# Performance work log

Measured on AMD Instinct MI355X. Metric: run time of the kernel, lower is better.

The kernel has to match this reference:

```python
import jax, jax.numpy as jnp
import numpy as np

NA = 3
ANCHORS = np.array([1.28967, 4.15014, 2.12714, 5.09344, 3.27212, 5.87423], dtype=np.float32)
OBJECT_SCALE = 5.0
NOOBJECT_SCALE = 1.0
CLASS_SCALE = 1.0
COORD_SCALE = 1.0
SIL_THRESH = 0.6
GAMMA = 0.5
EPS = 1e-7


def _iou_cxcywh(b1, b2):
    # b1, b2: [..., 4] as (cx, cy, w, h); broadcasting elementwise IoU
    mx = jnp.minimum(b1[..., 0] - b1[..., 2] * 0.5, b2[..., 0] - b2[..., 2] * 0.5)
    Mx = jnp.maximum(b1[..., 0] + b1[..., 2] * 0.5, b2[..., 0] + b2[..., 2] * 0.5)
    my = jnp.minimum(b1[..., 1] - b1[..., 3] * 0.5, b2[..., 1] - b2[..., 3] * 0.5)
    My = jnp.maximum(b1[..., 1] + b1[..., 3] * 0.5, b2[..., 1] + b2[..., 3] * 0.5)
    uw = Mx - mx
    uh = My - my
    cw = b1[..., 2] + b2[..., 2] - uw
    ch = b1[..., 3] + b2[..., 3] - uh
    inter = jnp.where((cw <= 0) | (ch <= 0), 0.0, cw * ch)
    union = b1[..., 2] * b1[..., 3] + b2[..., 2] * b2[..., 3] - inter
    return inter / union


def setup_inputs() -> dict:
    key = jax.random.key(0)
    k1, k2, k3, k4, k5 = jax.random.split(key, 5)
    nB, nC, nH, nW = 32, 80, 56, 56
    output = jax.random.normal(k1, (nB, NA * (5 + nC), nH, nW), dtype=jnp.float32)
    cxy = jax.random.uniform(k2, (nB, 50, 2), minval=0.02, maxval=0.98)
    wh = jax.random.uniform(k3, (nB, 50, 2), minval=0.05, maxval=0.6)
    target_boxes = jnp.concatenate([cxy, wh], axis=-1).astype(jnp.float32)
    target_cls = (jax.random.uniform(k4, (nB, 50, nC)) < 0.05).astype(jnp.float32)
    class_weight = jax.random.uniform(k5, (nC,), dtype=jnp.float32)
    return {"output": output, "target_boxes": target_boxes,
            "target_cls": target_cls, "class_weight": class_weight}


def reference(output, target_boxes, target_cls, class_weight):
    sg = jax.lax.stop_gradient
    anchors = jnp.asarray(ANCHORS)
    aw_all, ah_all = anchors[0::2], anchors[1::2]          # [nA]
    nB, _, nH, nW = output.shape
    nC = class_weight.shape[0]
    nA = NA
    out = output.reshape(nB, nA, 5 + nC, nH, nW)
    x = jax.nn.sigmoid(out[:, :, 0])                        # [nB,nA,nH,nW]
    y = jax.nn.sigmoid(out[:, :, 1])
    w = out[:, :, 2]
    h = out[:, :, 3]
    conf = jax.nn.sigmoid(out[:, :, 4])
    # class probs: [nB,nA,nH,nW,nC] (matches torch view/transpose to [nB*nA*nH*nW, nC])
    p_cls = jax.nn.sigmoid(jnp.transpose(out[:, :, 5:], (0, 1, 3, 4, 2)))

    grid_x = jnp.arange(nW, dtype=jnp.float32)[None, None, None, :]
    grid_y = jnp.arange(nH, dtype=jnp.float32)[None, None, :, None]
    # predicted boxes in grid units (detached, as torch uses .data)
    px = sg(x) + grid_x
    py = sg(y) + grid_y
    pw = jnp.exp(sg(w)) * aw_all[None, :, None, None]
    ph = jnp.exp(sg(h)) * ah_all[None, :, None, None]
    pred = jnp.stack([px, py, pw, ph], axis=-1).reshape(nB, nA * nH * nW, 4)

    # ---- build_targets (vectorized over (b, t, anchor*cell)) ----
    scale = jnp.array([nW, nH, nW, nH], dtype=jnp.float32)
    g = sg(target_boxes) * scale                            # [nB,50,4] grid units
    valid = target_boxes[:, :, 2] > 0                       # [nB,50]
    # IoU of every gt against every predicted box; max over gt -> silence mask
    ious = _iou_cxcywh(g[:, :, None, :], pred[:, None, :, :])  # [nB,50,nA*nH*nW]
    max_iou = jnp.max(jnp.where(valid[:, :, None], ious, 0.0), axis=1)
    conf_mask = jnp.where(max_iou > SIL_THRESH, 0.0, NOOBJECT_SCALE)  # [nB,nA*nH*nW]

    gx, gy, gw, gh = g[..., 0], g[..., 1], g[..., 2], g[..., 3]
    # best anchor by centered-box IoU: inter = min(w)*min(h)
    inter_a = jnp.minimum(aw_all, gw[..., None]) * jnp.minimum(ah_all, gh[..., None])
    union_a = aw_all * ah_all + (gw * gh)[..., None] - inter_a
    best_n = jnp.argmax(inter_a / union_a, axis=-1)         # [nB,50]

    gi = jnp.clip(gx.astype(jnp.int32), 0, nW - 1)
    gj = jnp.clip(gy.astype(jnp.int32), 0, nH - 1)
    b_idx = jnp.arange(nB)[:, None]
    flat = ((b_idx * nA + best_n) * nH + gj) * nW + gi      # [nB,50]
    total = nB * nA * nH * nW
    idx = jnp.where(valid, flat, total).reshape(-1)         # invalid -> out-of-range, dropped

    zeros = jnp.zeros((total,), dtype=jnp.float32)
    coord_mask = zeros.at[idx].set(1.0, mode="drop")
    conf_mask = conf_mask.reshape(-1).at[idx].set(OBJECT_SCALE, mode="drop")
    aw_b = aw_all[best_n]
    ah_b = ah_all[best_n]
    tx = zeros.at[idx].set((gx - gi.astype(jnp.float32)).reshape(-1), mode="drop")
    ty = zeros.at[idx].set((gy - gj.astype(jnp.float32)).reshape(-1), mode="drop")
    tw = zeros.at[idx].set(jnp.log(gw / aw_b).reshape(-1), mode="drop")
    th = zeros.at[idx].set(jnp.log(gh / ah_b).reshape(-1), mode="drop")
    pred_flat = pred.reshape(total, 4)
    pred_at = pred_flat[jnp.where(valid, flat, 0).reshape(-1)]  # [nB*50,4]
    iou_gt = _iou_cxcywh(g.reshape(-1, 4), pred_at)
    tconf = zeros.at[idx].set(iou_gt, mode="drop")
    tcls = jnp.zeros((total, nC), dtype=jnp.float32).at[idx].set(
        sg(target_cls).reshape(-1, nC), mode="drop")

    shp = (nB, nA, nH, nW)
    coord_mask = sg(coord_mask.reshape(shp))
    conf_mask = sg(conf_mask.reshape(shp))
    tx, ty, tw, th, tconf = (sg(t.reshape(shp)) for t in (tx, ty, tw, th, tconf))
    tcls = sg(tcls.reshape(nB, nA, nH, nW, nC))

    # ---- losses ----
    loss_x = 0.5 * COORD_SCALE * jnp.sum(coord_mask * (x - tx) ** 2)
    loss_y = 0.5 * COORD_SCALE * jnp.sum(coord_mask * (y - ty) ** 2)
    loss_w = 0.5 * COORD_SCALE * jnp.sum(coord_mask * (w - tw) ** 2)
    loss_h = 0.5 * COORD_SCALE * jnp.sum(coord_mask * (h - th) ** 2)
    # conf_mask is sqrt'ed then squared inside MSE -> equals conf_mask weighting
    loss_conf = 0.5 * jnp.sum(conf_mask * (conf - tconf) ** 2)

    # binary focal loss over cells selected by cls_mask (== coord_mask), size-averaged
    l1 = (1.0 - p_cls + EPS) ** GAMMA * jnp.log(p_cls + EPS) * jnp.exp(class_weight)
    l0 = (p_cls + EPS) ** GAMMA * jnp.log(1.0 - p_cls + EPS) * jnp.exp(1.0 - class_weight)
    per_el = tcls * l1 + (1.0 - tcls) * l0
    nsel = jnp.maximum(jnp.sum(coord_mask), 1.0)
    loss_cls = CLASS_SCALE * (-jnp.sum(coord_mask[..., None] * per_el) / nsel)

    return loss_x + loss_y + loss_w + loss_h + loss_conf + loss_cls
```

## Files before the change

### kernel.cpp

```cpp
#include <hip/hip_runtime.h>
#include <math.h>

#define NB 32
#define NA 3
#define NC 80
#define NH 56
#define NW 56
#define NT 50
#define HW (NH*NW)
#define CELLS_PER_B (NA*HW)
#define CH_PER_A (5+NC)
#define EPSF 1e-7f
#define NBX ((CELLS_PER_B + 255) / 256)
#define NBLK (NBX*NB)

__device__ __forceinline__ float fsig(float v) { return 1.0f / (1.0f + __expf(-v)); }

__global__ __launch_bounds__(256) void fused_kernel(const float* __restrict__ out,
                                                    const float* __restrict__ tb,
                                                    const float* __restrict__ tcls,
                                                    const float* __restrict__ cwt,
                                                    float4* __restrict__ part) {
    __shared__ float4 sp1[NT];
    __shared__ float2 sqf[NT];
    __shared__ int    s_obj[NT];
    __shared__ int    s_cnt;
    __shared__ float  redm[4], redc[4];

    const int b = blockIdx.y;
    const int tid = threadIdx.x;

    const float aw[3]  = {1.28967f, 2.12714f, 3.27212f};
    const float ah[3]  = {4.15014f, 5.09344f, 5.87423f};
    const float law[3] = {0.25438842f, 0.75477730f, 1.18543813f};
    const float lah[3] = {1.42314173f, 1.62795138f, 1.77057764f};

    if (tid == 0) s_cnt = 0;
    if (tid < NT) {
        float4 box = ((const float4*)tb)[b * NT + tid];
        if (box.z > 0.0f) {
            float gx = box.x * (float)NW;
            float gy = box.y * (float)NH;
            float gw = box.z * (float)NW;
            float gh = box.w * (float)NH;
            sp1[tid] = make_float4(gx - 0.5f * gw, gx + 0.5f * gw,
                                   gy - 0.5f * gh, gy + 0.5f * gh);
            int bn = 0; float best = -1.0f;
            #pragma unroll
            for (int k = 0; k < 3; ++k) {
                float inter = fminf(aw[k], gw) * fminf(ah[k], gh);
                float uni = aw[k] * ah[k] + gw * gh - inter;
                float r = inter / uni;
                if (r > best) { best = r; bn = k; }
            }
            int gi = (int)gx; gi = gi < 0 ? 0 : (gi > NW - 1 ? NW - 1 : gi);
            int gj = (int)gy; gj = gj < 0 ? 0 : (gj > NH - 1 ? NH - 1 : gj);
            int flat = (bn * NH + gj) * NW + gi;
            sqf[tid] = make_float2(0.375f * gw * gh, __int_as_float(flat));
        } else {
            sp1[tid] = make_float4(1e9f, -1e9f, 1e9f, -1e9f);
            sqf[tid] = make_float2(0.0f, __int_as_float(-1));
        }
    }
    __syncthreads();

    const int lc = blockIdx.x * 256 + tid;
    float lmain = 0.0f;

    if (lc < CELLS_PER_B) {
        const int a = lc / HW;
        const int rem = lc - a * HW;
        const int j = rem / NW;
        const int i = rem - j * NW;

        const float* base = out + (size_t)b * (NA * CH_PER_A * HW) + (size_t)(a * CH_PER_A) * HW + rem;
        float o0 = base[0];
        float o1 = base[HW];
        float o2 = base[2 * HW];
        float o3 = base[3 * HW];
        float o4 = base[4 * HW];

        float x = fsig(o0);
        float y = fsig(o1);
        float conf = fsig(o4);
        float pw = __expf(o2) * aw[a];
        float ph = __expf(o3) * ah[a];
        float px = x + (float)i;
        float py = y + (float)j;
        float px1 = px - 0.5f * pw, px2 = px + 0.5f * pw;
        float py1 = py - 0.5f * ph, py2 = py + 0.5f * ph;
        float qp = 0.375f * (pw * ph);

        bool sil = false;
        int tsel = -1;
        #pragma unroll 5
        for (int t = 0; t < NT; ++t) {
            float4 p1 = sp1[t];
            float2 qf = sqf[t];
            float iw = fminf(p1.y, px2) - fmaxf(p1.x, px1);
            float ih = fminf(p1.w, py2) - fmaxf(p1.z, py1);
            float in = fmaxf(iw, 0.f) * fmaxf(ih, 0.f);
            sil = sil || (in > qf.x + qp);
            if (__float_as_int(qf.y) == lc) tsel = t;
        }

        if (tsel >= 0) {
            float4 g1 = sp1[tsel];
            float gw = g1.y - g1.x, gh = g1.w - g1.z;
            float gx = 0.5f * (g1.x + g1.y), gy = 0.5f * (g1.z + g1.w);
            float tx = gx - (float)i, ty = gy - (float)j;
            float tw = __logf(gw) - law[a], th = __logf(gh) - lah[a];
            lmain += 0.5f * ((x - tx) * (x - tx) + (y - ty) * (y - ty) +
                             (o2 - tw) * (o2 - tw) + (o3 - th) * (o3 - th));
            float iw = fminf(g1.y, px2) - fmaxf(g1.x, px1);
            float ih = fminf(g1.w, py2) - fmaxf(g1.z, py1);
            float inter = fmaxf(iw, 0.f) * fmaxf(ih, 0.f);
            float uni = gw * gh + pw * ph - inter;
            float tconf = inter / uni;
            lmain += 2.5f * (conf - tconf) * (conf - tconf);

            int pos = atomicAdd(&s_cnt, 1);
            s_obj[pos] = (lc << 6) | tsel;
        } else {
            lmain += sil ? 0.0f : 0.5f * conf * conf;
        }
    }
    __syncthreads();

    const int cnt = s_cnt;
    float lcls = 0.0f;
    if (cnt > 0) {
        const int oo = tid / NC;
        const int c = tid - oo * NC;
        if (oo < 3) {
            float w = cwt[c];
            float ew1 = __expf(w);
            float ew0 = __expf(1.0f - w);
            for (int o0 = 0; o0 < cnt; o0 += 3) {
                int o = o0 + oo;
                if (o < cnt) {
                    int pk = s_obj[o];
                    int olc = pk >> 6;
                    int tsel = pk & 63;
                    int a = olc / HW;
                    int rem = olc - a * HW;
                    float p = fsig(out[(size_t)b * (NA * CH_PER_A * HW) +
                                       (size_t)(a * CH_PER_A + 5 + c) * HW + rem]);
                    float t = tcls[(size_t)(b * NT + tsel) * NC + c];
                    float l1 = sqrtf(1.0f - p + EPSF) * __logf(p + EPSF) * ew1;
                    float l0 = sqrtf(p + EPSF) * __logf(1.0f - p + EPSF) * ew0;
                    lcls += t * l1 + (1.0f - t) * l0;
                }
            }
        }
    }

    for (int off = 32; off > 0; off >>= 1) {
        lmain += __shfl_down(lmain, off, 64);
        lcls  += __shfl_down(lcls, off, 64);
    }
    if ((tid & 63) == 0) { redm[tid >> 6] = lmain; redc[tid >> 6] = lcls; }
    __syncthreads();
    if (tid == 0) {
        float m = redm[0] + redm[1] + redm[2] + redm[3];
        float c = redc[0] + redc[1] + redc[2] + redc[3];
        part[blockIdx.y * NBX + blockIdx.x] = make_float4(m, c, (float)cnt, 0.0f);
    }
}

__global__ __launch_bounds__(256) void finalize_kernel(const float4* __restrict__ part,
                                                       float* __restrict__ outp) {
    const int tid = threadIdx.x;
    float m = 0.0f, c = 0.0f, n = 0.0f;
    for (int i = tid; i < NBLK; i += 256) {
        float4 p = part[i];
        m += p.x; c += p.y; n += p.z;
    }
    for (int off = 32; off > 0; off >>= 1) {
        m += __shfl_down(m, off, 64);
        c += __shfl_down(c, off, 64);
        n += __shfl_down(n, off, 64);
    }
    __shared__ float rm[4], rc[4], rn[4];
    if ((tid & 63) == 0) { rm[tid >> 6] = m; rc[tid >> 6] = c; rn[tid >> 6] = n; }
    __syncthreads();
    if (tid == 0) {
        float ms = rm[0] + rm[1] + rm[2] + rm[3];
        float cs = rc[0] + rc[1] + rc[2] + rc[3];
        float ns = rn[0] + rn[1] + rn[2] + rn[3];
        float nsel = fmaxf(ns, 1.0f);
        outp[0] = ms - cs / nsel;
    }
}

extern "C" void kernel_launch(void* const* d_in, const int* in_sizes, int n_in,
                              void* d_out, int out_size, void* d_ws, size_t ws_size,
                              hipStream_t stream) {
    const float* output = (const float*)d_in[0];
    const float* tb     = (const float*)d_in[1];
    const float* tcls   = (const float*)d_in[2];
    const float* cwt    = (const float*)d_in[3];

    float4* part = (float4*)d_ws;

    fused_kernel<<<dim3(NBX, NB), 256, 0, stream>>>(output, tb, tcls, cwt, part);
    finalize_kernel<<<1, 256, 0, stream>>>(part, (float*)d_out);
}
```

Before: 20.19 us.

## Scatter target cell map in shared memory and issue class-prob loads early

Target-to-cell assignment now runs before the main IoU loop. Each target writes its index into a per-block shared map with atomicMax, which removes the per-cell comparison against every target's flat index inside the 50-iteration loop. Because the object list is known early, the first class-probability, target-class and class-weight loads are issued before the silence IoU loop, so their global-memory latency overlaps with that compute. The cost is two extra block barriers and some extra shared memory.

```diff
diff --git a/kernel.cpp b/kernel.cpp
--- a/kernel.cpp
+++ b/kernel.cpp
@@ -22,20 +22,41 @@
                                                     const float* __restrict__ cwt,
                                                     float4* __restrict__ part) {
     __shared__ float4 sp1[NT];
-    __shared__ float2 sqf[NT];
+    __shared__ float  sq[NT];
+    __shared__ int    s_map[256];
     __shared__ int    s_obj[NT];
     __shared__ int    s_cnt;
     __shared__ float  redm[4], redc[4];
 
     const int b = blockIdx.y;
     const int tid = threadIdx.x;
+    const int block_lo = blockIdx.x * 256;
+    const int lc = block_lo + tid;
+    const size_t bofs = (size_t)b * (NA * CH_PER_A * HW);
 
     const float aw[3]  = {1.28967f, 2.12714f, 3.27212f};
     const float ah[3]  = {4.15014f, 5.09344f, 5.87423f};
     const float law[3] = {0.25438842f, 0.75477730f, 1.18543813f};
     const float lah[3] = {1.42314173f, 1.62795138f, 1.77057764f};
 
+    const int a = lc / HW;
+    const int rem = lc - a * HW;
+    const int j = rem / NW;
+    const int i = rem - j * NW;
+    float o0 = 0.f, o1 = 0.f, o2 = 0.f, o3 = 0.f, o4 = 0.f;
+    const bool cv = (lc < CELLS_PER_B);
+    if (cv) {
+        const float* base = out + bofs + (size_t)(a * CH_PER_A) * HW + rem;
+        o0 = base[0];
+        o1 = base[HW];
+        o2 = base[2 * HW];
+        o3 = base[3 * HW];
+        o4 = base[4 * HW];
+    }
+
+    s_map[tid] = 0;
     if (tid == 0) s_cnt = 0;
+    int myflat = -1;
     if (tid < NT) {
         float4 box = ((const float4*)tb)[b * NT + tid];
         if (box.z > 0.0f) {
@@ -45,6 +66,7 @@
             float gh = box.w * (float)NH;
             sp1[tid] = make_float4(gx - 0.5f * gw, gx + 0.5f * gw,
                                    gy - 0.5f * gh, gy + 0.5f * gh);
+            sq[tid] = 0.375f * gw * gh;
             int bn = 0; float best = -1.0f;
             #pragma unroll
             for (int k = 0; k < 3; ++k) {
@@ -55,55 +77,67 @@
             }
             int gi = (int)gx; gi = gi < 0 ? 0 : (gi > NW - 1 ? NW - 1 : gi);
             int gj = (int)gy; gj = gj < 0 ? 0 : (gj > NH - 1 ? NH - 1 : gj);
-            int flat = (bn * NH + gj) * NW + gi;
-            sqf[tid] = make_float2(0.375f * gw * gh, __int_as_float(flat));
+            myflat = (bn * NH + gj) * NW + gi;
         } else {
             sp1[tid] = make_float4(1e9f, -1e9f, 1e9f, -1e9f);
-            sqf[tid] = make_float2(0.0f, __int_as_float(-1));
+            sq[tid] = 0.0f;
         }
     }
     __syncthreads();
-
-    const int lc = blockIdx.x * 256 + tid;
+    if (myflat >= block_lo && myflat < block_lo + 256)
+        atomicMax(&s_map[myflat - block_lo], tid + 1);
+    __syncthreads();
+
+    const int tsel = s_map[tid] - 1;
+    if (tsel >= 0) {
+        int pos = atomicAdd(&s_cnt, 1);
+        s_obj[pos] = (tid << 8) | tsel;
+    }
+    __syncthreads();
+
+    const int cnt = s_cnt;
+    const int oo = tid / NC;
+    const int cc = tid - oo * NC;
+    float praw = 0.f, traw = 0.f, wcls = 0.f;
+    bool gv = false;
+    int golc = 0;
+    if (oo < 3 && oo < cnt) {
+        int pk = s_obj[oo];
+        golc = block_lo + (pk >> 8);
+        int gts = pk & 255;
+        int ga = golc / HW;
+        int grem = golc - ga * HW;
+        praw = out[bofs + (size_t)(ga * CH_PER_A + 5 + cc) * HW + grem];
+        traw = tcls[(size_t)(b * NT + (pk & 255)) * NC + cc];
+        wcls = cwt[cc];
+        (void)gts;
+        gv = true;
+    }
+
+    float x = fsig(o0);
+    float y = fsig(o1);
+    float conf = fsig(o4);
+    float pw = __expf(o2) * aw[a < 3 ? a : 0];
+    float ph = __expf(o3) * ah[a < 3 ? a : 0];
+    float px = x + (float)i;
+    float py = y + (float)j;
+    float px1 = px - 0.5f * pw, px2 = px + 0.5f * pw;
+    float py1 = py - 0.5f * ph, py2 = py + 0.5f * ph;
+    float qp = 0.375f * (pw * ph);
+
+    bool sil = false;
+    #pragma unroll 5
+    for (int t = 0; t < NT; ++t) {
+        float4 p1 = sp1[t];
+        float qt = sq[t];
+        float iw = fminf(p1.y, px2) - fmaxf(p1.x, px1);
+        float ih = fminf(p1.w, py2) - fmaxf(p1.z, py1);
+        float in = fmaxf(iw, 0.f) * fmaxf(ih, 0.f);
+        sil = sil || (in > qt + qp);
+    }
+
     float lmain = 0.0f;
-
-    if (lc < CELLS_PER_B) {
-        const int a = lc / HW;
-        const int rem = lc - a * HW;
-        const int j = rem / NW;
-        const int i = rem - j * NW;
-
-        const float* base = out + (size_t)b * (NA * CH_PER_A * HW) + (size_t)(a * CH_PER_A) * HW + rem;
-        float o0 = base[0];
-        float o1 = base[HW];
-        float o2 = base[2 * HW];
-        float o3 = base[3 * HW];
-        float o4 = base[4 * HW];
-
-        float x = fsig(o0);
-        float y = fsig(o1);
-        float conf = fsig(o4);
-        float pw = __expf(o2) * aw[a];
-        float ph = __expf(o3) * ah[a];
-        float px = x + (float)i;
-        float py = y + (float)j;
-        float px1 = px - 0.5f * pw, px2 = px + 0.5f * pw;
-        float py1 = py - 0.5f * ph, py2 = py + 0.5f * ph;
-        float qp = 0.375f * (pw * ph);
-
-        bool sil = false;
-        int tsel = -1;
-        #pragma unroll 5
-        for (int t = 0; t < NT; ++t) {
-            float4 p1 = sp1[t];
-            float2 qf = sqf[t];
-            float iw = fminf(p1.y, px2) - fmaxf(p1.x, px1);
-            float ih = fminf(p1.w, py2) - fmaxf(p1.z, py1);
-            float in = fmaxf(iw, 0.f) * fmaxf(ih, 0.f);
-            sil = sil || (in > qf.x + qp);
-            if (__float_as_int(qf.y) == lc) tsel = t;
-        }
-
+    if (cv) {
         if (tsel >= 0) {
             float4 g1 = sp1[tsel];
             float gw = g1.y - g1.x, gh = g1.w - g1.z;
@@ -118,40 +152,32 @@
             float uni = gw * gh + pw * ph - inter;
             float tconf = inter / uni;
             lmain += 2.5f * (conf - tconf) * (conf - tconf);
-
-            int pos = atomicAdd(&s_cnt, 1);
-            s_obj[pos] = (lc << 6) | tsel;
         } else {
             lmain += sil ? 0.0f : 0.5f * conf * conf;
         }
     }
-    __syncthreads();
-
-    const int cnt = s_cnt;
+
     float lcls = 0.0f;
-    if (cnt > 0) {
-        const int oo = tid / NC;
-        const int c = tid - oo * NC;
-        if (oo < 3) {
-            float w = cwt[c];
-            float ew1 = __expf(w);
-            float ew0 = __expf(1.0f - w);
-            for (int o0 = 0; o0 < cnt; o0 += 3) {
-                int o = o0 + oo;
-                if (o < cnt) {
-                    int pk = s_obj[o];
-                    int olc = pk >> 6;
-                    int tsel = pk & 63;
-                    int a = olc / HW;
-                    int rem = olc - a * HW;
-                    float p = fsig(out[(size_t)b * (NA * CH_PER_A * HW) +
-                                       (size_t)(a * CH_PER_A + 5 + c) * HW + rem]);
-                    float t = tcls[(size_t)(b * NT + tsel) * NC + c];
-                    float l1 = sqrtf(1.0f - p + EPSF) * __logf(p + EPSF) * ew1;
-                    float l0 = sqrtf(p + EPSF) * __logf(1.0f - p + EPSF) * ew0;
-                    lcls += t * l1 + (1.0f - t) * l0;
-                }
-            }
+    if (gv) {
+        float p = fsig(praw);
+        float ew1 = __expf(wcls);
+        float ew0 = __expf(1.0f - wcls);
+        float l1 = sqrtf(1.0f - p + EPSF) * __logf(p + EPSF) * ew1;
+        float l0 = sqrtf(p + EPSF) * __logf(1.0f - p + EPSF) * ew0;
+        lcls += traw * l1 + (1.0f - traw) * l0;
+    }
+    if (oo < 3) {
+        for (int o = oo + 3; o < cnt; o += 3) {
+            int pk = s_obj[o];
+            int olc2 = block_lo + (pk >> 8);
+            int a2 = olc2 / HW;
+            int rem2 = olc2 - a2 * HW;
+            float p = fsig(out[bofs + (size_t)(a2 * CH_PER_A + 5 + cc) * HW + rem2]);
+            float t2 = tcls[(size_t)(b * NT + (pk & 255)) * NC + cc];
+            float w = cwt[cc];
+            float l1 = sqrtf(1.0f - p + EPSF) * __logf(p + EPSF) * __expf(w);
+            float l0 = sqrtf(p + EPSF) * __logf(1.0f - p + EPSF) * __expf(1.0f - w);
+            lcls += t2 * l1 + (1.0f - t2) * l0;
         }
     }
 
```

Result: faster. 19.18 us (-5.0%).
